# Performance work log

Hardware: AMD Instinct MI355X
Metric: run time of the kernel (lower is better)

The kernel has to match this reference:

```python
import jax, jax.numpy as jnp
import numpy as np

V, E, H, B, TE, TD = 32000, 256, 256, 32, 128, 64


def _gru_cell(x, h, Wi, Wh, bi, bh):
    # PyTorch GRU gate order: r, z, n
    gi = x @ Wi.T + bi            # [B, 3H]
    gh = h @ Wh.T + bh            # [B, 3H]
    i_r, i_z, i_n = jnp.split(gi, 3, axis=-1)
    h_r, h_z, h_n = jnp.split(gh, 3, axis=-1)
    r = jax.nn.sigmoid(i_r + h_r)
    z = jax.nn.sigmoid(i_z + h_z)
    n = jnp.tanh(i_n + r * h_n)
    return (1.0 - z) * n + z * h


def _run_gru(x_seq, h0, Wi, Wh, bi, bh, reverse=False):
    # x_seq: [B, T, D] -> outputs [B, T, H]
    xs = jnp.swapaxes(x_seq, 0, 1)  # [T, B, D]
    def step(h, x_t):
        h = _gru_cell(x_t, h, Wi, Wh, bi, bh)
        return h, h
    _, ys = jax.lax.scan(step, h0, xs, reverse=reverse)
    return jnp.swapaxes(ys, 0, 1)


def setup_inputs() -> dict:
    key = jax.random.key(0)
    ks = jax.random.split(key, 22)
    k = 1.0 / np.sqrt(H)
    u = lambda kk, shape, a: jax.random.uniform(kk, shape, jnp.float32, -a, a)
    return {
        'enc_in': jax.random.randint(ks[0], (B, TE), 0, V),
        'dec_in': jax.random.randint(ks[1], (B, TD), 0, V),
        'embed_W': u(ks[2], (V, E), 0.1),
        'Wi_f': u(ks[3], (3 * H, E), k), 'Wh_f': u(ks[4], (3 * H, H), k),
        'bi_f': u(ks[5], (3 * H,), k), 'bh_f': u(ks[6], (3 * H,), k),
        'Wi_b': u(ks[7], (3 * H, E), k), 'Wh_b': u(ks[8], (3 * H, H), k),
        'bi_b': u(ks[9], (3 * H,), k), 'bh_b': u(ks[10], (3 * H,), k),
        'Wi_d': u(ks[11], (3 * H, E + 2 * H), k), 'Wh_d': u(ks[12], (3 * H, H), k),
        'bi_d': u(ks[13], (3 * H,), k), 'bh_d': u(ks[14], (3 * H,), k),
        'W1_w': u(ks[15], (H, 2 * H), 1.0 / np.sqrt(2 * H)), 'W1_b': u(ks[16], (H,), 1.0 / np.sqrt(2 * H)),
        'W2_w': u(ks[17], (2 * H, H), k), 'W2_b': u(ks[18], (2 * H,), k),
        'lin_w': u(ks[19], (V, H), 0.1), 'lin_b': jnp.zeros((V,), jnp.float32),
    }


def reference(enc_in, dec_in, embed_W, Wi_f, Wh_f, bi_f, bh_f, Wi_b, Wh_b, bi_b, bh_b,
              Wi_d, Wh_d, bi_d, bh_d, W1_w, W1_b, W2_w, W2_b, lin_w, lin_b):
    # ---- encoder (bidirectional GRU, 1 layer) ----
    enc_emb = embed_W[enc_in]                                   # [B, TE, E]
    h0 = jnp.zeros((B, H), enc_emb.dtype)
    out_f = _run_gru(enc_emb, h0, Wi_f, Wh_f, bi_f, bh_f)       # [B, TE, H]
    out_b = _run_gru(enc_emb, h0, Wi_b, Wh_b, bi_b, bh_b, reverse=True)
    encoded = jnp.concatenate([out_f, out_b], axis=-1)          # [B, TE, 2H]

    # last valid state per example: encoded[i, sizes[i]-1]
    sizes = (enc_in > 0).sum(axis=1)                            # [B]
    last_states = encoded[jnp.arange(B), sizes - 1]             # [B, 2H]

    # ---- decoder with Luong attention (teacher forcing) ----
    dec_emb = embed_W[dec_in]                                   # [B, TD, E]
    h_init = last_states @ W1_w.T + W1_b                        # [B, H]
    ctx_init = jnp.zeros((B, 2 * H), enc_emb.dtype)

    def dec_step(carry, x_t):
        h, ctx = carry
        inp = jnp.concatenate([ctx, x_t], axis=-1)              # [B, E+2H]
        h = _gru_cell(inp, h, Wi_d, Wh_d, bi_d, bh_d)           # [B, H]
        comp = h @ W2_w.T + W2_b                                # [B, 2H]
        scores = jax.nn.softmax(jnp.einsum('bte,be->bt', encoded, comp), axis=-1)
        ctx = jnp.einsum('bt,bte->be', scores, encoded)          # [B, 2H]
        return (h, ctx), h

    _, outs = jax.lax.scan(dec_step, (h_init, ctx_init), jnp.swapaxes(dec_emb, 0, 1))
    outs = jnp.swapaxes(outs, 0, 1)                             # [B, TD, H]
    logits = outs @ lin_w.T + lin_b                             # [B, TD, V]
    return logits
```

## Files before the change

kernel.cpp:

```cpp
#include <hip/hip_runtime.h>
#include <hip/hip_bf16.h>

#define Vv 32000
#define Ee 256
#define Hh 256
#define Bb 32
#define TEe 128
#define TDd 64

typedef __attribute__((ext_vector_type(4))) float f32x4;
typedef __attribute__((ext_vector_type(8))) short short8;
typedef __attribute__((ext_vector_type(2))) unsigned int uint2v;
typedef __attribute__((ext_vector_type(4))) unsigned int uint4v;

static __device__ __forceinline__ unsigned short f2bf(float f){
  unsigned u = __float_as_uint(f);
  u += 0x7fffu + ((u >> 16) & 1u);
  return (unsigned short)(u >> 16);
}
static __device__ __forceinline__ unsigned pack2(float a, float b){
  return ((unsigned)f2bf(b) << 16) | (unsigned)f2bf(a);
}
static __device__ __forceinline__ float dot8(uint4v u, const float* hh){
  float s = 0.f;
  #pragma unroll
  for (int i = 0; i < 4; ++i){
    unsigned w = u[i];
    s = fmaf(__uint_as_float(w << 16),        hh[2*i],   s);
    s = fmaf(__uint_as_float(w & 0xffff0000u), hh[2*i+1], s);
  }
  return s;
}
static __device__ __forceinline__ float sigmoidf_(float x){
  return 1.f / (1.f + __expf(-x));
}

__global__ void k_sizes(const int* __restrict__ enc_in, int* __restrict__ sizes){
  int b = threadIdx.x;
  if (b < Bb){
    int c = 0;
    for (int t = 0; t < TEe; ++t) c += (enc_in[b*TEe + t] > 0);
    sizes[b] = c;
  }
}

__global__ void k_gather(const int* __restrict__ tok, const float* __restrict__ embW,
                         float* __restrict__ out, int rows){
  int i = blockIdx.x * 256 + threadIdx.x;
  int r = i >> 8, c = i & 255;
  if (r < rows) out[i] = embW[(size_t)tok[r]*Ee + c];
}

__global__ void k_extract_bf16(const float* __restrict__ src, unsigned short* __restrict__ dst,
                               int n){
  int i = blockIdx.x * 256 + threadIdx.x;
  if (i < n) dst[i] = f2bf(src[i]);
}

__global__ void k_chunkw(const float* __restrict__ src, unsigned short* __restrict__ dst, int rows){
  int idx = blockIdx.x * 256 + threadIdx.x;
  if (idx < rows * 256){
    int i = idx & 7, r = (idx >> 3) % rows, kb = idx / (rows * 8);
    dst[idx] = f2bf(src[(size_t)r*256 + kb*8 + i]);
  }
}

__global__ void k_projchunk(const float* __restrict__ in, unsigned short* __restrict__ out){
  int idx = blockIdx.x * 256 + threadIdx.x;
  int i = idx & 7;
  int t1 = idx >> 3;
  int n = t1 % 768;
  int t2 = t1 / 768;
  int kb = t2 & 15, b = t2 >> 4;
  out[idx] = f2bf(in[(size_t)(b*TEe + kb*8 + i)*768 + n]);
}

template<bool A_BF16, bool B_BF16, bool B_KMAJOR, bool OUT_BF16>
__global__ __launch_bounds__(256) void k_gemm(
  const void* __restrict__ Av, const void* __restrict__ Bv,
  const float* __restrict__ bias, void* __restrict__ Cv,
  int M, int N, int K, int lda, int ldb, int ldc)
{
  __shared__ unsigned short lA[128*40];
  __shared__ unsigned short lB[128*40];
  const int tid  = threadIdx.x;
  const int lane = tid & 63;
  const int w = tid >> 6, wr = w >> 1, wc = w & 1;
  const int m0 = blockIdx.y * 128, n0 = blockIdx.x * 128;
  f32x4 acc[4][4];
  #pragma unroll
  for (int i = 0; i < 4; ++i)
    #pragma unroll
    for (int j = 0; j < 4; ++j) acc[i][j] = (f32x4){0.f,0.f,0.f,0.f};

  for (int k0 = 0; k0 < K; k0 += 32){
    if (A_BF16){
      const unsigned short* A = (const unsigned short*)Av;
      #pragma unroll
      for (int it = 0; it < 2; ++it){
        int idx = tid + it*256; int r = idx >> 2, q = idx & 3;
        *(uint4v*)&lA[r*40 + q*8] = *(const uint4v*)(A + (size_t)(m0+r)*lda + k0 + q*8);
      }
    } else {
      const float* A = (const float*)Av;
      #pragma unroll
      for (int it = 0; it < 4; ++it){
        int idx = tid + it*256; int r = idx >> 3, q = idx & 7;
        f32x4 v = *(const f32x4*)(A + (size_t)(m0+r)*lda + k0 + q*4);
        uint2v pk; pk[0] = pack2(v[0], v[1]); pk[1] = pack2(v[2], v[3]);
        *(uint2v*)&lA[r*40 + q*4] = pk;
      }
    }
    if (B_KMAJOR){
      const float* Bp = (const float*)Bv;
      #pragma unroll
      for (int it = 0; it < 4; ++it){
        int idx = tid + it*256; int kk = idx >> 5, nq = idx & 31;
        f32x4 v = *(const f32x4*)(Bp + (size_t)(k0+kk)*ldb + n0 + nq*4);
        #pragma unroll
        for (int s2 = 0; s2 < 4; ++s2) lB[(nq*4+s2)*40 + kk] = f2bf(v[s2]);
      }
    } else if (B_BF16){
      const unsigned short* Bp = (const unsigned short*)Bv;
      #pragma unroll
      for (int it = 0; it < 2; ++it){
        int idx = tid + it*256; int r = idx >> 2, q = idx & 3;
        *(uint4v*)&lB[r*40 + q*8] = *(const uint4v*)(Bp + (size_t)(n0+r)*ldb + k0 + q*8);
      }
    } else {
      const float* Bp = (const float*)Bv;
      #pragma unroll
      for (int it = 0; it < 4; ++it){
        int idx = tid + it*256; int r = idx >> 3, q = idx & 7;
        f32x4 v = *(const f32x4*)(Bp + (size_t)(n0+r)*ldb + k0 + q*4);
        uint2v pk; pk[0] = pack2(v[0], v[1]); pk[1] = pack2(v[2], v[3]);
        *(uint2v*)&lB[r*40 + q*4] = pk;
      }
    }
    __syncthreads();
    short8 av[4], bv[4];
    #pragma unroll
    for (int i = 0; i < 4; ++i)
      av[i] = *(const short8*)&lA[(wr*64 + i*16 + (lane&15))*40 + (lane>>4)*8];
    #pragma unroll
    for (int j = 0; j < 4; ++j)
      bv[j] = *(const short8*)&lB[(wc*64 + j*16 + (lane&15))*40 + (lane>>4)*8];
    #pragma unroll
    for (int i = 0; i < 4; ++i)
      #pragma unroll
      for (int j = 0; j < 4; ++j)
        acc[i][j] = __builtin_amdgcn_mfma_f32_16x16x32_bf16(av[i], bv[j], acc[i][j], 0, 0, 0);
    __syncthreads();
  }
  #pragma unroll
  for (int i = 0; i < 4; ++i){
    #pragma unroll
    for (int j = 0; j < 4; ++j){
      int col = n0 + wc*64 + j*16 + (lane & 15);
      float bb = bias ? bias[col] : 0.f;
      #pragma unroll
      for (int r = 0; r < 4; ++r){
        int row = m0 + wr*64 + i*16 + (lane>>4)*4 + r;
        float v = acc[i][j][r] + bb;
        if (OUT_BF16) ((unsigned short*)Cv)[(size_t)row*ldc + col] = f2bf(v);
        else          ((float*)Cv)[(size_t)row*ldc + col] = v;
      }
    }
  }
}

__global__ __launch_bounds__(512, 1) void k_encoder(
  const unsigned short* __restrict__ Whf, const unsigned short* __restrict__ Whb,
  const float* __restrict__ bhf, const float* __restrict__ bhb,
  const float* __restrict__ gif, const float* __restrict__ gib,
  float* __restrict__ encoded)
{
  extern __shared__ char smem[];
  unsigned short* lw = (unsigned short*)smem;
  float* hA   = (float*)(smem + 131072);
  float* hB   = (float*)(smem + 132096);
  float* parL = (float*)(smem + 133120);
  float* parS = (float*)(smem + 135168);
  const int dir = blockIdx.x & 1, b = blockIdx.x >> 1;
  const unsigned short* Wh = dir ? Whb : Whf;
  const float* bh = dir ? bhb : bhf;
  const float* gi = dir ? gib : gif;
  const int T = threadIdx.x;
  const int rL = T >> 1, hfq = (T & 1)*16;
  const unsigned short* wsrc = Wh + (size_t)(256 + T)*8;
  uint4v wb[8];
  #pragma unroll
  for (int d = 0; d < 8; ++d) wb[d] = *(const uint4v*)(wsrc + (size_t)d*6144);
  for (int cc = T; cc < 256*32; cc += 512){
    int r = cc >> 5, q = cc & 31;
    *(uint4v*)&lw[(r*32 + (q ^ (r & 31)))*8] = *(const uint4v*)(Wh + (size_t)q*6144 + r*8);
  }
  float bh0 = 0.f, bh1 = 0.f, bh2 = 0.f;
  if (T < 256){ bh0 = bh[T]; bh1 = bh[T+256]; bh2 = bh[T+512]; hA[T] = 0.f; }
  __syncthreads();
  const float* hc = hA; float* hn = hB;
  for (int s = 0; s < TEe; ++s){
    const int t = dir ? (TEe-1-s) : s;
    {
      const unsigned short* lwr = lw + rL*256;
      float a = 0.f;
      #pragma unroll
      for (int i = 0; i < 16; ++i){
        const int q = hfq + i;
        float hr[8];
        *(f32x4*)&hr[0] = *(const f32x4*)&hc[q*8];
        *(f32x4*)&hr[4] = *(const f32x4*)&hc[q*8+4];
        a += dot8(*(const uint4v*)(lwr + ((q ^ (rL & 31)) << 3)), hr);
      }
      parL[(T & 1)*256 + rL] = a;
    }
    {
      float a = 0.f;
      #pragma unroll
      for (int q = 0; q < 32; ++q){
        float hr[8];
        *(f32x4*)&hr[0] = *(const f32x4*)&hc[q*8];
        *(f32x4*)&hr[4] = *(const f32x4*)&hc[q*8+4];
        a += dot8(wb[q & 7], hr);
        wb[q & 7] = *(const uint4v*)(wsrc + (size_t)((q < 24) ? (q + 8) : (q - 24))*6144);
      }
      parS[T] = a;
    }
    __syncthreads();
    if (T < 256){
      const int j = T;
      const float* grow = gi + (size_t)(b*TEe + t)*768;
      const float A0 = parL[j] + parL[256+j] + bh0;
      const float A1 = parS[j] + bh1;
      const float A2 = parS[256+j] + bh2;
      const float r = sigmoidf_(grow[j] + A0);
      const float z = sigmoidf_(grow[j+256] + A1);
      const float n = tanhf(grow[j+512] + r*A2);
      const float hnew = (1.f - z)*n + z*hc[j];
      hn[j] = hnew;
      encoded[(size_t)(b*TEe + t)*512 + dir*256 + j] = hnew;
    }
    __syncthreads();
    const float* tmp = hc; hc = hn; hn = (float*)tmp;
  }
}

__global__ void k_encb2(const float* __restrict__ encoded, const float* __restrict__ W2b,
                        float* __restrict__ encb2){
  int r = blockIdx.x, l = threadIdx.x;
  const float* e = encoded + (size_t)r*512;
  float s = 0.f;
  for (int k = l; k < 512; k += 64) s += e[k]*W2b[k];
  for (int off = 32; off; off >>= 1) s += __shfl_down(s, off);
  if (l == 0) encb2[r] = s;
}

__global__ void k_hinit(const float* __restrict__ encoded, const int* __restrict__ sizes,
                        const float* __restrict__ W1w, const float* __restrict__ W1b,
                        float* __restrict__ h0){
  int b = blockIdx.x, o = threadIdx.x;
  int idx = sizes[b] - 1;
  idx = idx < 0 ? 0 : (idx > TEe-1 ? TEe-1 : idx);
  const float* ls = encoded + (size_t)(b*TEe + idx)*512;
  const float* wv = W1w + (size_t)o*512;
  float s = W1b[o];
  for (int k = 0; k < 512; k += 4){
    f32x4 a = *(const f32x4*)(ls + k);
    f32x4 w4 = *(const f32x4*)(wv + k);
    s = fmaf(a[0],w4[0], fmaf(a[1],w4[1], fmaf(a[2],w4[2], fmaf(a[3],w4[3], s))));
  }
  h0[b*256 + o] = s;
}

#define DLR 128
__global__ __launch_bounds__(512, 1) void k_decoder(
  const unsigned short* __restrict__ Whd, const float* __restrict__ bhd,
  const float* __restrict__ gidx,
  const unsigned short* __restrict__ encw2,
  const float* __restrict__ encb2,
  const unsigned short* __restrict__ projt,
  const float* __restrict__ h0,
  unsigned short* __restrict__ outs_bf)
{
  extern __shared__ char smem[];
  unsigned short* le = (unsigned short*)smem;
  unsigned short* lw = (unsigned short*)(smem + 65536);
  float* h    = (float*)(smem + 131072);
  float* parL = (float*)(smem + 132096);
  float* parS1= (float*)(smem + 134144);
  float* parS2= (float*)(smem + 136192);
  float* gcs  = (float*)(smem + 138240);
  float* cpar = (float*)(smem + 140288);
  float* p    = (float*)(smem + 142336);
  float* ebl  = (float*)(smem + 142848);
  const int b = blockIdx.x, T = threadIdx.x;
  const unsigned short* ptc = projt + (size_t)b*98304;
  const unsigned short* wsrcM = Whd + (size_t)(DLR + T)*8;
  const int trow = 640 + (T >> 2), tq = (T & 3)*8;
  const unsigned short* wsrcT = Whd + (size_t)trow*8;
  const unsigned short* csrcM = ptc + (size_t)T*8;
  const int crow = 512 + (T >> 1), cq = (T & 1)*8;
  const unsigned short* csrcT = ptc + (size_t)crow*8;
  uint4v wb[8], wb2[2], cb[4], cb2[2];
  #pragma unroll
  for (int d = 0; d < 8; ++d) wb[d] = *(const uint4v*)(wsrcM + (size_t)d*6144);
  wb2[0] = *(const uint4v*)(wsrcT + (size_t)tq*6144);
  wb2[1] = *(const uint4v*)(wsrcT + (size_t)(tq+1)*6144);
  #pragma unroll
  for (int d = 0; d < 4; ++d) cb[d] = *(const uint4v*)(csrcM + (size_t)d*6144);
  cb2[0] = *(const uint4v*)(csrcT + (size_t)cq*6144);
  cb2[1] = *(const uint4v*)(csrcT + (size_t)(cq+1)*6144);
  for (int cc = T; cc < 128*32; cc += 512){
    int r = cc >> 5, q = cc & 31;
    *(uint4v*)&le[(r*32 + (q ^ (r & 31)))*8] =
        *(const uint4v*)(encw2 + ((size_t)(b*TEe + r) << 8) + (q << 3));
  }
  for (int cc = T; cc < DLR*32; cc += 512){
    int r = cc >> 5, q = cc & 31;
    *(uint4v*)&lw[(r*32 + (q ^ (r & 31)))*8] =
        *(const uint4v*)(Whd + (size_t)q*6144 + r*8);
  }
  for (int i = T; i < 256; i += 512) h[i] = h0[b*256 + i];
  gcs[T] = 0.f; cpar[T] = 0.f;
  if (T < TEe) ebl[T] = encb2[b*TEe + T];
  float bh0 = 0.f, bh1 = 0.f, bh2 = 0.f;
  if (T < 256){ bh0 = bhd[T]; bh1 = bhd[T+256]; bh2 = bhd[T+512]; }
  __syncthreads();
  float g0 = 0.f, g1 = 0.f, g2 = 0.f;
  if (T < 256){
    const float* grow = gidx + (size_t)(b*TDd)*768;
    g0 = grow[T]; g1 = grow[T+256]; g2 = grow[T+512];
  }
  #define DOTS_BODY                                                            \
  {                                                                            \
    { const int rL2 = T >> 2, qb = (T & 3)*8;                                  \
      const unsigned short* lwr = lw + rL2*256;                                \
      float a = 0.f;                                                           \
      _Pragma("unroll")                                                        \
      for (int i = 0; i < 8; ++i){                                             \
        const int q = qb + i;                                                  \
        float hr[8];                                                           \
        *(f32x4*)&hr[0] = *(const f32x4*)&h[q*8];                              \
        *(f32x4*)&hr[4] = *(const f32x4*)&h[q*8+4];                            \
        a += dot8(*(const uint4v*)(lwr + ((q ^ (rL2 & 31)) << 3)), hr);        \
      }                                                                        \
      parL[(T & 3)*128 + rL2] = a;                                             \
    }                                                                          \
    { float a = 0.f;                                                           \
      _Pragma("unroll")                                                        \
      for (int q = 0; q < 32; ++q){                                            \
        float hr[8];                                                           \
        *(f32x4*)&hr[0] = *(const f32x4*)&h[q*8];                              \
        *(f32x4*)&hr[4] = *(const f32x4*)&h[q*8+4];                            \
        a += dot8(wb[q & 7], hr);                                              \
        wb[q & 7] = *(const uint4v*)(wsrcM + (size_t)((q < 24) ? (q + 8) : (q - 24))*6144); \
      }                                                                        \
      parS1[T] = a;                                                            \
    }                                                                          \
    { float a = 0.f;                                                           \
      _Pragma("unroll")                                                        \
      for (int i = 0; i < 8; ++i){                                             \
        const int q = tq + i;                                                  \
        float hr[8];                                                           \
        *(f32x4*)&hr[0] = *(const f32x4*)&h[q*8];                              \
        *(f32x4*)&hr[4] = *(const f32x4*)&h[q*8+4];                            \
        a += dot8(wb2[i & 1], hr);                                             \
        wb2[i & 1] = *(const uint4v*)(wsrcT + (size_t)(tq + ((i < 6) ? (i + 2) : (i - 6)))*6144); \
      }                                                                        \
      parS2[(T & 3)*128 + (T >> 2)] = a;                                       \
    }                                                                          \
  }
  DOTS_BODY
  __syncthreads();
  for (int t = 0; t < TDd; ++t){
    if (T < 256){
      const int j = T;
      float A0, A2;
      if (j < 128){
        A0 = parL[j] + parL[128+j] + parL[256+j] + parL[384+j];
        A2 = parS1[384+j];
      } else {
        A0 = parS1[j-128];
        A2 = parS2[j-128] + parS2[j] + parS2[j+128] + parS2[j+256];
      }
      const float A1 = parS1[128+j];
      const float gcr = gcs[j];
      const float gcz = gcs[256+j];
      const float gcn = cpar[j] + cpar[256+j];
      const float r = sigmoidf_(g0 + gcr + A0 + bh0);
      const float z = sigmoidf_(g1 + gcz + A1 + bh1);
      const float n = tanhf(g2 + gcn + r*(A2 + bh2));
      const float hnew = (1.f - z)*n + z*h[j];
      h[j] = hnew;
      outs_bf[(size_t)(b*TDd + t)*256 + j] = f2bf(hnew);
    }
    if (t + 1 == TDd) break;
    __syncthreads();
    if (T < 256){
      const float* grow = gidx + (size_t)(b*TDd + t + 1)*768;
      g0 = grow[T]; g1 = grow[T+256]; g2 = grow[T+512];
    }
    DOTS_BODY
    {
      const int pos = T >> 2, kq = (T & 3)*8;
      const unsigned short* er = le + pos*256;
      float s = 0.f;
      #pragma unroll
      for (int i = 0; i < 8; ++i){
        const int q = kq + i;
        float hr[8];
        *(f32x4*)&hr[0] = *(const f32x4*)&h[q*8];
        *(f32x4*)&hr[4] = *(const f32x4*)&h[q*8+4];
        s += dot8(*(const uint4v*)(er + ((q ^ (pos & 31)) << 3)), hr);
      }
      s += __shfl_xor(s, 1);
      s += __shfl_xor(s, 2);
      if ((T & 3) == 0) p[pos] = s + ebl[pos];
    }
    __syncthreads();
    if (T < 64){
      float m = fmaxf(p[T], p[T+64]);
      for (int off = 32; off; off >>= 1) m = fmaxf(m, __shfl_xor(m, off));
      float e0 = __expf(p[T] - m), e1 = __expf(p[T+64] - m);
      float ss = e0 + e1;
      for (int off = 32; off; off >>= 1) ss += __shfl_xor(ss, off);
      float inv = 1.f / ss;
      p[T] = e0*inv; p[T+64] = e1*inv;
    }
    __syncthreads();
    {
      float c = 0.f;
      #pragma unroll
      for (int q = 0; q < 16; ++q){
        float pr[8];
        *(f32x4*)&pr[0] = *(const f32x4*)&p[q*8];
        *(f32x4*)&pr[4] = *(const f32x4*)&p[q*8+4];
        c += dot8(cb[q & 3], pr);
        cb[q & 3] = *(const uint4v*)(csrcM + (size_t)((q < 12) ? (q + 4) : (q - 12))*6144);
      }
      gcs[T] = c;
      float c2 = 0.f;
      #pragma unroll
      for (int i = 0; i < 8; ++i){
        const int q = cq + i;
        float pr[8];
        *(f32x4*)&pr[0] = *(const f32x4*)&p[q*8];
        *(f32x4*)&pr[4] = *(const f32x4*)&p[q*8+4];
        c2 += dot8(cb2[i & 1], pr);
        cb2[i & 1] = *(const uint4v*)(csrcT + (size_t)(cq + ((i < 6) ? (i + 2) : (i - 6)))*6144);
      }
      cpar[(T & 1)*256 + (T >> 1)] = c2;
    }
    __syncthreads();
  }
  #undef DOTS_BODY
}

extern "C" void kernel_launch(void* const* d_in, const int* in_sizes, int n_in,
                              void* d_out, int out_size, void* d_ws, size_t ws_size,
                              hipStream_t stream)
{
  (void)in_sizes; (void)n_in; (void)out_size;
  const int*   enc_in = (const int*)d_in[0];
  const int*   dec_in = (const int*)d_in[1];
  const float* embW   = (const float*)d_in[2];
  const float* Wi_f   = (const float*)d_in[3];
  const float* Wh_f   = (const float*)d_in[4];
  const float* bi_f   = (const float*)d_in[5];
  const float* bh_f   = (const float*)d_in[6];
  const float* Wi_b   = (const float*)d_in[7];
  const float* Wh_b   = (const float*)d_in[8];
  const float* bi_b   = (const float*)d_in[9];
  const float* bh_b   = (const float*)d_in[10];
  const float* Wi_d   = (const float*)d_in[11];
  const float* Wh_d   = (const float*)d_in[12];
  const float* bi_d   = (const float*)d_in[13];
  const float* bh_d   = (const float*)d_in[14];
  const float* W1_w   = (const float*)d_in[15];
  const float* W1_b   = (const float*)d_in[16];
  const float* W2_w   = (const float*)d_in[17];
  const float* W2_b   = (const float*)d_in[18];
  const float* lin_w  = (const float*)d_in[19];
  const float* lin_b  = (const float*)d_in[20];

  char* scr = (char*)d_out;
  float* emb_enc = (float*)(scr + 0);
  float* emb_dec = (float*)(scr + 4194304);
  float* gi_f    = (float*)(scr + 6291456);
  float* gi_b    = (float*)(scr + 18874368);
  float* gi_dx   = (float*)(scr + 31457280);
  float* enc     = (float*)(scr + 37748736);
  float* projf   = (float*)(scr + 46137344);
  unsigned short* whf_bf = (unsigned short*)(scr + 58720256);
  unsigned short* whb_bf = (unsigned short*)(scr + 59113472);
  unsigned short* whd_bf = (unsigned short*)(scr + 59506688);
  unsigned short* encw2  = (unsigned short*)(scr + 59899904);
  unsigned short* projt  = (unsigned short*)(scr + 61997056);
  float* encb2 = (float*)(scr + 68288512);
  int*   sizes = (int*)(scr + 68304896);
  float* h0    = (float*)(scr + 68305024);

  unsigned short* outs_bf = (unsigned short*)d_ws;
  unsigned short* lin_bf  = (unsigned short*)((char*)d_ws + (1<<20));
  const bool big = ws_size >= (size_t)(1<<20) + 16384000u + 1024u;

  hipFuncSetAttribute((const void*)k_encoder, hipFuncAttributeMaxDynamicSharedMemorySize, 137216);
  hipFuncSetAttribute((const void*)k_decoder, hipFuncAttributeMaxDynamicSharedMemorySize, 143360);

  k_sizes<<<1, 32, 0, stream>>>(enc_in, sizes);
  k_gather<<<Bb*TEe, 256, 0, stream>>>(enc_in, embW, emb_enc, Bb*TEe);
  k_gather<<<Bb*TDd, 256, 0, stream>>>(dec_in, embW, emb_dec, Bb*TDd);
  k_chunkw<<<768, 256, 0, stream>>>(Wh_f, whf_bf, 768);
  k_chunkw<<<768, 256, 0, stream>>>(Wh_b, whb_bf, 768);
  k_chunkw<<<768, 256, 0, stream>>>(Wh_d, whd_bf, 768);
  if (big) k_extract_bf16<<<32000, 256, 0, stream>>>(lin_w, lin_bf, 32000*256);

  k_gemm<false,false,false,false><<<dim3(6,32), 256, 0, stream>>>(
      emb_enc, Wi_f, bi_f, gi_f, 4096, 768, 256, 256, 256, 768);
  k_gemm<false,false,false,false><<<dim3(6,32), 256, 0, stream>>>(
      emb_enc, Wi_b, bi_b, gi_b, 4096, 768, 256, 256, 256, 768);
  k_gemm<false,false,false,false><<<dim3(6,16), 256, 0, stream>>>(
      emb_dec, Wi_d + 512, bi_d, gi_dx, 2048, 768, 256, 256, 768, 768);

  k_encoder<<<64, 512, 137216, stream>>>(whf_bf, whb_bf, bh_f, bh_b, gi_f, gi_b, enc);
  k_encb2<<<Bb*TEe, 64, 0, stream>>>(enc, W2_b, encb2);

  k_gemm<false,false,true,true><<<dim3(2,32), 256, 0, stream>>>(
      enc, W2_w, nullptr, encw2, 4096, 256, 512, 512, 256, 256);
  k_gemm<false,false,false,false><<<dim3(6,32), 256, 0, stream>>>(
      enc, Wi_d, nullptr, projf, 4096, 768, 512, 512, 768, 768);
  k_projchunk<<<(Bb*16*768*8)/256, 256, 0, stream>>>(projf, projt);
  k_hinit<<<Bb, 256, 0, stream>>>(enc, sizes, W1_w, W1_b, h0);

  k_decoder<<<Bb, 512, 143360, stream>>>(whd_bf, bh_d, gi_dx, encw2, encb2, projt, h0, outs_bf);

  if (big)
    k_gemm<true,true,false,false><<<dim3(250,16), 256, 0, stream>>>(
        outs_bf, lin_bf, lin_b, d_out, 2048, 32000, 256, 256, 256, 32000);
  else
    k_gemm<true,false,false,false><<<dim3(250,16), 256, 0, stream>>>(
        outs_bf, lin_w, lin_b, d_out, 2048, 32000, 256, 256, 256, 32000);
}
```

Before: 1.994 ms.

## Double encoder GRU block to 1024 threads, splitting recurrent matvec K across threads

The bidirectional encoder recurrence kernel now launches 1024 threads per block instead of 512. The LDS-resident r-gate rows are split four ways along K, and the register-resident z/n rows are split two ways along K, with partial sums combined in the gate stage. This halves the per-thread serial dot-product work on the latency-bound recurrent step, at the cost of more partial-sum shared memory, a larger reduction and higher register pressure under the 1024-thread launch bound.

```diff
diff --git a/kernel.cpp b/kernel.cpp
--- a/kernel.cpp
+++ b/kernel.cpp
@@ -169,7 +169,7 @@
   }
 }
 
-__global__ __launch_bounds__(512, 1) void k_encoder(
+__global__ __launch_bounds__(1024) void k_encoder(
   const unsigned short* __restrict__ Whf, const unsigned short* __restrict__ Whb,
   const float* __restrict__ bhf, const float* __restrict__ bhb,
   const float* __restrict__ gif, const float* __restrict__ gib,
@@ -179,19 +179,20 @@
   unsigned short* lw = (unsigned short*)smem;
   float* hA   = (float*)(smem + 131072);
   float* hB   = (float*)(smem + 132096);
-  float* parL = (float*)(smem + 133120);
-  float* parS = (float*)(smem + 135168);
+  float* parA = (float*)(smem + 133120);
+  float* parB = (float*)(smem + 137216);
   const int dir = blockIdx.x & 1, b = blockIdx.x >> 1;
   const unsigned short* Wh = dir ? Whb : Whf;
   const float* bh = dir ? bhb : bhf;
   const float* gi = dir ? gib : gif;
   const int T = threadIdx.x;
-  const int rL = T >> 1, hfq = (T & 1)*16;
-  const unsigned short* wsrc = Wh + (size_t)(256 + T)*8;
+  const int rl = T & 255, q4 = T >> 8;
+  const int rrh = T & 511, hf = T >> 9;
+  const unsigned short* wsrc = Wh + (size_t)(hf*16)*6144 + (size_t)(256 + rrh)*8;
   uint4v wb[8];
   #pragma unroll
   for (int d = 0; d < 8; ++d) wb[d] = *(const uint4v*)(wsrc + (size_t)d*6144);
-  for (int cc = T; cc < 256*32; cc += 512){
+  for (int cc = T; cc < 256*32; cc += 1024){
     int r = cc >> 5, q = cc & 31;
     *(uint4v*)&lw[(r*32 + (q ^ (r & 31)))*8] = *(const uint4v*)(Wh + (size_t)q*6144 + r*8);
   }
@@ -201,38 +202,34 @@
   const float* hc = hA; float* hn = hB;
   for (int s = 0; s < TEe; ++s){
     const int t = dir ? (TEe-1-s) : s;
-    {
-      const unsigned short* lwr = lw + rL*256;
-      float a = 0.f;
-      #pragma unroll
-      for (int i = 0; i < 16; ++i){
-        const int q = hfq + i;
-        float hr[8];
-        *(f32x4*)&hr[0] = *(const f32x4*)&hc[q*8];
-        *(f32x4*)&hr[4] = *(const f32x4*)&hc[q*8+4];
-        a += dot8(*(const uint4v*)(lwr + ((q ^ (rL & 31)) << 3)), hr);
-      }
-      parL[(T & 1)*256 + rL] = a;
-    }
-    {
-      float a = 0.f;
-      #pragma unroll
-      for (int q = 0; q < 32; ++q){
-        float hr[8];
-        *(f32x4*)&hr[0] = *(const f32x4*)&hc[q*8];
-        *(f32x4*)&hr[4] = *(const f32x4*)&hc[q*8+4];
-        a += dot8(wb[q & 7], hr);
-        wb[q & 7] = *(const uint4v*)(wsrc + (size_t)((q < 24) ? (q + 8) : (q - 24))*6144);
-      }
-      parS[T] = a;
-    }
+    float aL = 0.f;
+    #pragma unroll
+    for (int i = 0; i < 8; ++i){
+      const int ck = q4*8 + i;
+      float hr[8];
+      *(f32x4*)&hr[0] = *(const f32x4*)&hc[ck*8];
+      *(f32x4*)&hr[4] = *(const f32x4*)&hc[ck*8+4];
+      aL += dot8(*(const uint4v*)&lw[(rl*32 + (ck ^ (rl & 31)))*8], hr);
+    }
+    parA[q4*256 + rl] = aL;
+    float aR = 0.f;
+    const float* hh = hc + hf*128;
+    #pragma unroll
+    for (int q = 0; q < 16; ++q){
+      float hr[8];
+      *(f32x4*)&hr[0] = *(const f32x4*)&hh[q*8];
+      *(f32x4*)&hr[4] = *(const f32x4*)&hh[q*8+4];
+      aR += dot8(wb[q & 7], hr);
+      wb[q & 7] = *(const uint4v*)(wsrc + (size_t)((q < 8) ? (q + 8) : (q - 8))*6144);
+    }
+    parB[hf*512 + rrh] = aR;
     __syncthreads();
     if (T < 256){
       const int j = T;
       const float* grow = gi + (size_t)(b*TEe + t)*768;
-      const float A0 = parL[j] + parL[256+j] + bh0;
-      const float A1 = parS[j] + bh1;
-      const float A2 = parS[256+j] + bh2;
+      const float A0 = parA[j] + parA[256+j] + parA[512+j] + parA[768+j] + bh0;
+      const float A1 = parB[j] + parB[512+j] + bh1;
+      const float A2 = parB[256+j] + parB[768+j] + bh2;
       const float r = sigmoidf_(grow[j] + A0);
       const float z = sigmoidf_(grow[j+256] + A1);
       const float n = tanhf(grow[j+512] + r*A2);
@@ -504,7 +501,7 @@
   unsigned short* lin_bf  = (unsigned short*)((char*)d_ws + (1<<20));
   const bool big = ws_size >= (size_t)(1<<20) + 16384000u + 1024u;
 
-  hipFuncSetAttribute((const void*)k_encoder, hipFuncAttributeMaxDynamicSharedMemorySize, 137216);
+  hipFuncSetAttribute((const void*)k_encoder, hipFuncAttributeMaxDynamicSharedMemorySize, 141312);
   hipFuncSetAttribute((const void*)k_decoder, hipFuncAttributeMaxDynamicSharedMemorySize, 143360);
 
   k_sizes<<<1, 32, 0, stream>>>(enc_in, sizes);
@@ -522,7 +519,7 @@
   k_gemm<false,false,false,false><<<dim3(6,16), 256, 0, stream>>>(
       emb_dec, Wi_d + 512, bi_d, gi_dx, 2048, 768, 256, 256, 768, 768);
 
-  k_encoder<<<64, 512, 137216, stream>>>(whf_bf, whb_bf, bh_f, bh_b, gi_f, gi_b, enc);
+  k_encoder<<<64, 1024, 141312, stream>>>(whf_bf, whb_bf, bh_f, bh_b, gi_f, gi_b, enc);
   k_encb2<<<Bb*TEe, 64, 0, stream>>>(enc, W2_b, encb2);
 
   k_gemm<false,false,true,true><<<dim3(2,32), 256, 0, stream>>>(
```

Result: faster. 1.703 ms (-14.6%).

## Overlap lin_w bf16 conversion with encoder recurrence; single h buffer in encoder

Applied to the files above, without the earlier changes.

The separate lin_w fp32-to-bf16 conversion kernel is removed. Its work is folded into 128 extra blocks of the encoder launch, so the conversion runs on otherwise idle CUs while the 64 latency-bound recurrence blocks execute. The encoder LDS matvec is also re-split so each thread handles two rows over 8 chunks with a four-way partial sum, and the double-buffered hidden state becomes a single buffer. The extra blocks request the same large dynamic LDS, which limits them to one block per CU. The in-place h update also relies on every thread having read h before the first barrier.

```diff
diff --git a/kernel.cpp b/kernel.cpp
--- a/kernel.cpp
+++ b/kernel.cpp
@@ -173,20 +173,28 @@
   const unsigned short* __restrict__ Whf, const unsigned short* __restrict__ Whb,
   const float* __restrict__ bhf, const float* __restrict__ bhb,
   const float* __restrict__ gif, const float* __restrict__ gib,
-  float* __restrict__ encoded)
+  float* __restrict__ encoded,
+  const float* __restrict__ lin_w, unsigned short* __restrict__ lin_bf, int do_lin)
 {
+  if (blockIdx.x >= 64){
+    if (do_lin){
+      const int nlin = Vv*Hh;
+      for (int i = (blockIdx.x - 64)*512 + threadIdx.x; i < nlin; i += 128*512)
+        lin_bf[i] = f2bf(lin_w[i]);
+    }
+    return;
+  }
   extern __shared__ char smem[];
   unsigned short* lw = (unsigned short*)smem;
-  float* hA   = (float*)(smem + 131072);
-  float* hB   = (float*)(smem + 132096);
-  float* parL = (float*)(smem + 133120);
-  float* parS = (float*)(smem + 135168);
+  float* h    = (float*)(smem + 131072);
+  float* parL = (float*)(smem + 132096);
+  float* parS = (float*)(smem + 136192);
   const int dir = blockIdx.x & 1, b = blockIdx.x >> 1;
   const unsigned short* Wh = dir ? Whb : Whf;
   const float* bh = dir ? bhb : bhf;
   const float* gi = dir ? gib : gif;
   const int T = threadIdx.x;
-  const int rL = T >> 1, hfq = (T & 1)*16;
+  const int rA = T & 127, rB = rA + 128, qb = (T >> 7)*8;
   const unsigned short* wsrc = Wh + (size_t)(256 + T)*8;
   uint4v wb[8];
   #pragma unroll
@@ -196,31 +204,33 @@
     *(uint4v*)&lw[(r*32 + (q ^ (r & 31)))*8] = *(const uint4v*)(Wh + (size_t)q*6144 + r*8);
   }
   float bh0 = 0.f, bh1 = 0.f, bh2 = 0.f;
-  if (T < 256){ bh0 = bh[T]; bh1 = bh[T+256]; bh2 = bh[T+512]; hA[T] = 0.f; }
+  if (T < 256){ bh0 = bh[T]; bh1 = bh[T+256]; bh2 = bh[T+512]; h[T] = 0.f; }
   __syncthreads();
-  const float* hc = hA; float* hn = hB;
   for (int s = 0; s < TEe; ++s){
     const int t = dir ? (TEe-1-s) : s;
     {
-      const unsigned short* lwr = lw + rL*256;
-      float a = 0.f;
-      #pragma unroll
-      for (int i = 0; i < 16; ++i){
-        const int q = hfq + i;
+      const unsigned short* lwA = lw + rA*256;
+      const unsigned short* lwB = lw + rB*256;
+      float a1 = 0.f, a2 = 0.f;
+      #pragma unroll
+      for (int i = 0; i < 8; ++i){
+        const int q = qb + i;
         float hr[8];
-        *(f32x4*)&hr[0] = *(const f32x4*)&hc[q*8];
-        *(f32x4*)&hr[4] = *(const f32x4*)&hc[q*8+4];
-        a += dot8(*(const uint4v*)(lwr + ((q ^ (rL & 31)) << 3)), hr);
-      }
-      parL[(T & 1)*256 + rL] = a;
+        *(f32x4*)&hr[0] = *(const f32x4*)&h[q*8];
+        *(f32x4*)&hr[4] = *(const f32x4*)&h[q*8+4];
+        a1 += dot8(*(const uint4v*)(lwA + ((q ^ (rA & 31)) << 3)), hr);
+        a2 += dot8(*(const uint4v*)(lwB + ((q ^ (rB & 31)) << 3)), hr);
+      }
+      parL[(T >> 7)*256 + rA] = a1;
+      parL[(T >> 7)*256 + rB] = a2;
     }
     {
       float a = 0.f;
       #pragma unroll
       for (int q = 0; q < 32; ++q){
         float hr[8];
-        *(f32x4*)&hr[0] = *(const f32x4*)&hc[q*8];
-        *(f32x4*)&hr[4] = *(const f32x4*)&hc[q*8+4];
+        *(f32x4*)&hr[0] = *(const f32x4*)&h[q*8];
+        *(f32x4*)&hr[4] = *(const f32x4*)&h[q*8+4];
         a += dot8(wb[q & 7], hr);
         wb[q & 7] = *(const uint4v*)(wsrc + (size_t)((q < 24) ? (q + 8) : (q - 24))*6144);
       }
@@ -230,18 +240,17 @@
     if (T < 256){
       const int j = T;
       const float* grow = gi + (size_t)(b*TEe + t)*768;
-      const float A0 = parL[j] + parL[256+j] + bh0;
+      const float A0 = parL[j] + parL[256+j] + parL[512+j] + parL[768+j] + bh0;
       const float A1 = parS[j] + bh1;
       const float A2 = parS[256+j] + bh2;
       const float r = sigmoidf_(grow[j] + A0);
       const float z = sigmoidf_(grow[j+256] + A1);
       const float n = tanhf(grow[j+512] + r*A2);
-      const float hnew = (1.f - z)*n + z*hc[j];
-      hn[j] = hnew;
+      const float hnew = (1.f - z)*n + z*h[j];
+      h[j] = hnew;
       encoded[(size_t)(b*TEe + t)*512 + dir*256 + j] = hnew;
     }
     __syncthreads();
-    const float* tmp = hc; hc = hn; hn = (float*)tmp;
   }
 }
 
@@ -333,12 +342,12 @@
   }
   #define DOTS_BODY                                                            \
   {                                                                            \
-    { const int rL2 = T >> 2, qb = (T & 3)*8;                                  \
+    { const int rL2 = T >> 2, qb2 = (T & 3)*8;                                 \
       const unsigned short* lwr = lw + rL2*256;                                \
       float a = 0.f;                                                           \
       _Pragma("unroll")                                                        \
       for (int i = 0; i < 8; ++i){                                             \
-        const int q = qb + i;                                                  \
+        const int q = qb2 + i;                                                 \
         float hr[8];                                                           \
         *(f32x4*)&hr[0] = *(const f32x4*)&h[q*8];                              \
         *(f32x4*)&hr[4] = *(const f32x4*)&h[q*8+4];                            \
@@ -504,7 +513,7 @@
   unsigned short* lin_bf  = (unsigned short*)((char*)d_ws + (1<<20));
   const bool big = ws_size >= (size_t)(1<<20) + 16384000u + 1024u;
 
-  hipFuncSetAttribute((const void*)k_encoder, hipFuncAttributeMaxDynamicSharedMemorySize, 137216);
+  hipFuncSetAttribute((const void*)k_encoder, hipFuncAttributeMaxDynamicSharedMemorySize, 138240);
   hipFuncSetAttribute((const void*)k_decoder, hipFuncAttributeMaxDynamicSharedMemorySize, 143360);
 
   k_sizes<<<1, 32, 0, stream>>>(enc_in, sizes);
@@ -513,7 +522,6 @@
   k_chunkw<<<768, 256, 0, stream>>>(Wh_f, whf_bf, 768);
   k_chunkw<<<768, 256, 0, stream>>>(Wh_b, whb_bf, 768);
   k_chunkw<<<768, 256, 0, stream>>>(Wh_d, whd_bf, 768);
-  if (big) k_extract_bf16<<<32000, 256, 0, stream>>>(lin_w, lin_bf, 32000*256);
 
   k_gemm<false,false,false,false><<<dim3(6,32), 256, 0, stream>>>(
       emb_enc, Wi_f, bi_f, gi_f, 4096, 768, 256, 256, 256, 768);
@@ -522,7 +530,8 @@
   k_gemm<false,false,false,false><<<dim3(6,16), 256, 0, stream>>>(
       emb_dec, Wi_d + 512, bi_d, gi_dx, 2048, 768, 256, 256, 768, 768);
 
-  k_encoder<<<64, 512, 137216, stream>>>(whf_bf, whb_bf, bh_f, bh_b, gi_f, gi_b, enc);
+  k_encoder<<<192, 512, 138240, stream>>>(whf_bf, whb_bf, bh_f, bh_b, gi_f, gi_b,
+                                          enc, lin_w, lin_bf, big ? 1 : 0);
   k_encb2<<<Bb*TEe, 64, 0, stream>>>(enc, W2_b, encb2);
 
   k_gemm<false,false,true,true><<<dim3(2,32), 256, 0, stream>>>(
```

Result: faster. 1.783 ms (-10.6%).
